# Optimization experiments

Hardware: AMD Instinct MI355X
Metric: run time of the kernel (lower is better)

## Reference

```python
import jax, jax.numpy as jnp
import numpy as np

N, NW, M, H, C = 16384, 512, 32, 8, 16
T_SEG, N_SIG = 512, 3


def _forward(query_feats, key_feats, value_feats, query_table, key_table,
             value_table, table_offsets, win_indices, table_idx):
    # gather voxels into windows: [nW, M, H, C]
    q = query_feats[win_indices]
    k = key_feats[win_indices]
    v = value_feats[win_indices]
    # base attention coefficients: [nW, H, M, M]
    logits = jnp.einsum('wihc,wjhc->whij', q, k)
    n_sig = table_idx.shape[-1]
    for s in range(n_sig):  # fixed, small signal loop (xyz cRSE)
        idx_s = table_offsets[s] + table_idx[..., s]      # [nW, M, M]
        tq = query_table[idx_s]                            # [nW, M, M, H, C]
        tk = key_table[idx_s]
        logits = logits + jnp.einsum('wihc,wijhc->whij', q, tq) \
                        + jnp.einsum('wjhc,wijhc->whij', k, tk)
    # max-stabilized exp (cal_max_coffs + self_attn_forward)
    rmax = jnp.max(logits, axis=-1, keepdims=True)
    ecoff = jnp.exp(logits - rmax)                         # [nW, H, M, M]
    sum_coffs = jnp.sum(ecoff, axis=-1)                    # [nW, H, M]
    raw = jnp.einsum('whij,wjhc->wihc', ecoff, v)          # [nW, M, H, C]
    for s in range(n_sig):
        idx_s = table_offsets[s] + table_idx[..., s]
        tv = value_table[idx_s]
        raw = raw + jnp.einsum('whij,wijhc->wihc', ecoff, tv)
    norm = raw / jnp.transpose(sum_coffs, (0, 2, 1))[..., None]
    # scatter windows back to voxel order (win_indices is a permutation)
    out = jnp.zeros_like(query_feats).at[win_indices.reshape(-1)].set(
        norm.reshape(-1, norm.shape[-2], norm.shape[-1]))
    return out


def setup_inputs() -> dict:
    key = jax.random.key(0)
    ks = jax.random.split(key, 9)
    feats = lambda k: jax.random.normal(k, (N, H, C), dtype=jnp.float32)
    table = lambda k: 0.02 * jax.random.normal(k, (N_SIG * T_SEG, H, C), dtype=jnp.float32)
    win_indices = jax.random.permutation(ks[6], N).reshape(NW, M).astype(jnp.int32)
    table_idx = jax.random.randint(ks[7], (NW, M, M, N_SIG), 0, T_SEG, dtype=jnp.int32)
    table_offsets = (jnp.arange(N_SIG, dtype=jnp.int32) * T_SEG)
    return {
        'query_feats': feats(ks[0]), 'key_feats': feats(ks[1]), 'value_feats': feats(ks[2]),
        'query_table': table(ks[3]), 'key_table': table(ks[4]), 'value_table': table(ks[5]),
        'table_offsets': table_offsets, 'win_indices': win_indices, 'table_idx': table_idx,
    }


def reference(query_feats, key_feats, value_feats, query_table, key_table,
              value_table, table_offsets, win_indices, table_idx):
    return _forward(query_feats, key_feats, value_feats, query_table, key_table,
                    value_table, table_offsets, win_indices, table_idx)
```

## Files before the change

kernel.cpp:

```cpp
#include <hip/hip_runtime.h>

namespace {
constexpr int NWIN = 512;
constexpr int M    = 32;
constexpr int H    = 8;
constexpr int C    = 16;
constexpr int NSIG = 3;
constexpr int HC   = H * C;
constexpr int HB   = 4;
constexpr int HBC  = HB * C;
}

__device__ __forceinline__ float dot4(const float4& a, const float4& b) {
  return a.x * b.x + a.y * b.y + a.z * b.z + a.w * b.w;
}
__device__ __forceinline__ const float4* f4p(const float* p) {
  return reinterpret_cast<const float4*>(p);
}

__global__ __launch_bounds__(256, 4)
void win_attn(const float* __restrict__ qf, const float* __restrict__ kf,
              const float* __restrict__ vf, const float* __restrict__ qt,
              const float* __restrict__ kt, const float* __restrict__ vt,
              const int* __restrict__ toff, const int* __restrict__ widx,
              const int* __restrict__ tidx, float* __restrict__ out)
{
  const int w  = blockIdx.x >> 1;
  const int hb = (blockIdx.x & 1) * HB;
  const int t  = threadIdx.x;
  const int hl = t >> 6;
  const int ch = (t >> 5) & 1;
  const int i  = t & 31;
  const int h  = hb + hl;
  const int cb = ch * 8;

  __shared__ float k_lds[M][HBC];
  __shared__ float v_lds[M][HBC];
  __shared__ int   tid_lds[M * NSIG * M];
  __shared__ int   vox_lds[M];
  __shared__ int   off_lds[NSIG];

  if (t < M)    vox_lds[t] = widx[w * M + t];
  if (t < NSIG) off_lds[t] = toff[t];
  __syncthreads();

  #pragma unroll
  for (int r = 0; r < 2; ++r) {
    const int flat = t + 256 * r;
    const int j    = flat >> 4;
    const int f4i  = (flat & 15) * 4;
    const int goff = vox_lds[j] * HC + hb * C + f4i;
    *reinterpret_cast<float4*>(&k_lds[j][f4i]) = *f4p(kf + goff);
    *reinterpret_cast<float4*>(&v_lds[j][f4i]) = *f4p(vf + goff);
  }
  #pragma unroll
  for (int r = 0; r < 12; ++r) {
    const int g   = t + 256 * r;
    const int ii  = g / 96;
    const int rem = g - ii * 96;
    const int jj  = rem / 3;
    const int ss  = rem - jj * 3;
    tid_lds[(jj * NSIG + ss) * M + ii] = tidx[w * (M * M * NSIG) + g];
  }

  const int vox_i = vox_lds[i];
  const float* qrow = qf + vox_i * HC + h * C + cb;
  const float4 q0 = f4p(qrow)[0], q1 = f4p(qrow)[1];
  const int offs[NSIG] = { off_lds[0], off_lds[1], off_lds[2] };
  __syncthreads();

  float m    = -INFINITY;
  float ssum = 0.f;
  float oacc[8];
  #pragma unroll
  for (int c = 0; c < 8; ++c) oacc[c] = 0.f;

  #pragma unroll
  for (int j = 0; j < M; ++j) {
    const float* krow = &k_lds[j][hl * C + cb];
    const float4 k0 = f4p(krow)[0], k1 = f4p(krow)[1];
    const float4 vv0 = f4p(&v_lds[j][hl * C + cb])[0];
    const float4 vv1 = f4p(&v_lds[j][hl * C + cb])[1];

    float logit = dot4(q0, k0) + dot4(q1, k1);
    float4 tv0[NSIG], tv1[NSIG];
    #pragma unroll
    for (int s = 0; s < NSIG; ++s) {
      const int row = offs[s] + tid_lds[(j * NSIG + s) * M + i];
      const float* base = qt + row * HC + h * C + cb;
      const float4 a0 = f4p(base)[0], a1 = f4p(base)[1];
      const float* kbase = kt + row * HC + h * C + cb;
      const float4 b0 = f4p(kbase)[0], b1 = f4p(kbase)[1];
      const float* vbase = vt + row * HC + h * C + cb;
      tv0[s] = f4p(vbase)[0];
      tv1[s] = f4p(vbase)[1];
      logit += dot4(q0, a0) + dot4(q1, a1) + dot4(k0, b0) + dot4(k1, b1);
    }
    logit += __shfl_xor(logit, 32);

    const float mnew  = fmaxf(m, logit);
    const float scale = expf(m - mnew);
    const float e     = expf(logit - mnew);
    ssum = ssum * scale + e;
    m    = mnew;

    float4 sv0 = tv0[0], sv1 = tv1[0];
    sv0.x += tv0[1].x + tv0[2].x + vv0.x;  sv0.y += tv0[1].y + tv0[2].y + vv0.y;
    sv0.z += tv0[1].z + tv0[2].z + vv0.z;  sv0.w += tv0[1].w + tv0[2].w + vv0.w;
    sv1.x += tv1[1].x + tv1[2].x + vv1.x;  sv1.y += tv1[1].y + tv1[2].y + vv1.y;
    sv1.z += tv1[1].z + tv1[2].z + vv1.z;  sv1.w += tv1[1].w + tv1[2].w + vv1.w;

    oacc[0] = oacc[0] * scale + e * sv0.x;
    oacc[1] = oacc[1] * scale + e * sv0.y;
    oacc[2] = oacc[2] * scale + e * sv0.z;
    oacc[3] = oacc[3] * scale + e * sv0.w;
    oacc[4] = oacc[4] * scale + e * sv1.x;
    oacc[5] = oacc[5] * scale + e * sv1.y;
    oacc[6] = oacc[6] * scale + e * sv1.z;
    oacc[7] = oacc[7] * scale + e * sv1.w;
  }

  const float inv = 1.0f / ssum;
  float* orow = out + vox_i * HC + h * C + cb;
  float4 o0, o1;
  o0.x = oacc[0] * inv;  o0.y = oacc[1] * inv;
  o0.z = oacc[2] * inv;  o0.w = oacc[3] * inv;
  o1.x = oacc[4] * inv;  o1.y = oacc[5] * inv;
  o1.z = oacc[6] * inv;  o1.w = oacc[7] * inv;
  reinterpret_cast<float4*>(orow)[0] = o0;
  reinterpret_cast<float4*>(orow)[1] = o1;
}

extern "C" void kernel_launch(void* const* d_in, const int* in_sizes, int n_in,
                              void* d_out, int out_size, void* d_ws, size_t ws_size,
                              hipStream_t stream) {
  (void)in_sizes; (void)n_in; (void)d_ws; (void)ws_size; (void)out_size;
  const float* qf  = (const float*)d_in[0];
  const float* kf  = (const float*)d_in[1];
  const float* vf  = (const float*)d_in[2];
  const float* qt  = (const float*)d_in[3];
  const float* kt  = (const float*)d_in[4];
  const float* vt  = (const float*)d_in[5];
  const int*  toff = (const int*)d_in[6];
  const int*  widx = (const int*)d_in[7];
  const int*  tidx = (const int*)d_in[8];
  float* out = (float*)d_out;
  win_attn<<<NWIN * 2, 256, 0, stream>>>(qf, kf, vf, qt, kt, vt, toff, widx, tidx, out);
}
```

Before: 351.7 us.

## Double-buffer gathered table rows in registers across key iterations

Splits the per-key loop into a load phase and a consume phase. Each step issues the table-row gathers for the next key into a second register buffer before working on the current key, so global-memory latency overlaps with the arithmetic. To make room for the two 18-float4 buffers, the launch bound drops from 4 to 2 waves-per-SIMD hint, which allows more registers per thread but risks lower occupancy.

```diff
diff --git a/kernel.cpp b/kernel.cpp
--- a/kernel.cpp
+++ b/kernel.cpp
@@ -18,7 +18,9 @@
   return reinterpret_cast<const float4*>(p);
 }
 
-__global__ __launch_bounds__(256, 4)
+struct RowBuf { float4 d[18]; };
+
+__global__ __launch_bounds__(256, 2)
 void win_attn(const float* __restrict__ qf, const float* __restrict__ kf,
               const float* __restrict__ vf, const float* __restrict__ qt,
               const float* __restrict__ kt, const float* __restrict__ vt,
@@ -33,6 +35,8 @@
   const int i  = t & 31;
   const int h  = hb + hl;
   const int cb = ch * 8;
+  const int hcb = h * C + cb;
+  const int lcb = hl * C + cb;
 
   __shared__ float k_lds[M][HBC];
   __shared__ float v_lds[M][HBC];
@@ -64,7 +68,7 @@
   }
 
   const int vox_i = vox_lds[i];
-  const float* qrow = qf + vox_i * HC + h * C + cb;
+  const float* qrow = qf + vox_i * HC + hcb;
   const float4 q0 = f4p(qrow)[0], q1 = f4p(qrow)[1];
   const int offs[NSIG] = { off_lds[0], off_lds[1], off_lds[2] };
   __syncthreads();
@@ -75,26 +79,30 @@
   #pragma unroll
   for (int c = 0; c < 8; ++c) oacc[c] = 0.f;
 
-  #pragma unroll
-  for (int j = 0; j < M; ++j) {
-    const float* krow = &k_lds[j][hl * C + cb];
-    const float4 k0 = f4p(krow)[0], k1 = f4p(krow)[1];
-    const float4 vv0 = f4p(&v_lds[j][hl * C + cb])[0];
-    const float4 vv1 = f4p(&v_lds[j][hl * C + cb])[1];
-
-    float logit = dot4(q0, k0) + dot4(q1, k1);
-    float4 tv0[NSIG], tv1[NSIG];
+  auto load_rows = [&](RowBuf& b, int j) {
     #pragma unroll
     for (int s = 0; s < NSIG; ++s) {
       const int row = offs[s] + tid_lds[(j * NSIG + s) * M + i];
-      const float* base = qt + row * HC + h * C + cb;
-      const float4 a0 = f4p(base)[0], a1 = f4p(base)[1];
-      const float* kbase = kt + row * HC + h * C + cb;
-      const float4 b0 = f4p(kbase)[0], b1 = f4p(kbase)[1];
-      const float* vbase = vt + row * HC + h * C + cb;
-      tv0[s] = f4p(vbase)[0];
-      tv1[s] = f4p(vbase)[1];
-      logit += dot4(q0, a0) + dot4(q1, a1) + dot4(k0, b0) + dot4(k1, b1);
+      const float* bq = qt + row * HC + hcb;
+      const float* bk = kt + row * HC + hcb;
+      const float* bv = vt + row * HC + hcb;
+      b.d[s * 6 + 0] = f4p(bq)[0];  b.d[s * 6 + 1] = f4p(bq)[1];
+      b.d[s * 6 + 2] = f4p(bk)[0];  b.d[s * 6 + 3] = f4p(bk)[1];
+      b.d[s * 6 + 4] = f4p(bv)[0];  b.d[s * 6 + 5] = f4p(bv)[1];
+    }
+  };
+
+  auto consume = [&](const RowBuf& b, int j) {
+    const float* krow = &k_lds[j][lcb];
+    const float4 k0 = f4p(krow)[0], k1 = f4p(krow)[1];
+    const float* vrow = &v_lds[j][lcb];
+    const float4 vv0 = f4p(vrow)[0], vv1 = f4p(vrow)[1];
+
+    float logit = dot4(q0, k0) + dot4(q1, k1);
+    #pragma unroll
+    for (int s = 0; s < NSIG; ++s) {
+      logit += dot4(q0, b.d[s * 6 + 0]) + dot4(q1, b.d[s * 6 + 1])
+             + dot4(k0, b.d[s * 6 + 2]) + dot4(k1, b.d[s * 6 + 3]);
     }
     logit += __shfl_xor(logit, 32);
 
@@ -104,12 +112,14 @@
     ssum = ssum * scale + e;
     m    = mnew;
 
-    float4 sv0 = tv0[0], sv1 = tv1[0];
-    sv0.x += tv0[1].x + tv0[2].x + vv0.x;  sv0.y += tv0[1].y + tv0[2].y + vv0.y;
-    sv0.z += tv0[1].z + tv0[2].z + vv0.z;  sv0.w += tv0[1].w + tv0[2].w + vv0.w;
-    sv1.x += tv1[1].x + tv1[2].x + vv1.x;  sv1.y += tv1[1].y + tv1[2].y + vv1.y;
-    sv1.z += tv1[1].z + tv1[2].z + vv1.z;  sv1.w += tv1[1].w + tv1[2].w + vv1.w;
-
+    float4 sv0 = vv0, sv1 = vv1;
+    #pragma unroll
+    for (int s = 0; s < NSIG; ++s) {
+      sv0.x += b.d[s * 6 + 4].x;  sv0.y += b.d[s * 6 + 4].y;
+      sv0.z += b.d[s * 6 + 4].z;  sv0.w += b.d[s * 6 + 4].w;
+      sv1.x += b.d[s * 6 + 5].x;  sv1.y += b.d[s * 6 + 5].y;
+      sv1.z += b.d[s * 6 + 5].z;  sv1.w += b.d[s * 6 + 5].w;
+    }
     oacc[0] = oacc[0] * scale + e * sv0.x;
     oacc[1] = oacc[1] * scale + e * sv0.y;
     oacc[2] = oacc[2] * scale + e * sv0.z;
@@ -118,10 +128,20 @@
     oacc[5] = oacc[5] * scale + e * sv1.y;
     oacc[6] = oacc[6] * scale + e * sv1.z;
     oacc[7] = oacc[7] * scale + e * sv1.w;
+  };
+
+  RowBuf A, B;
+  load_rows(A, 0);
+  #pragma unroll
+  for (int jj = 0; jj < M / 2; ++jj) {
+    load_rows(B, 2 * jj + 1);
+    consume(A, 2 * jj);
+    if (jj < M / 2 - 1) load_rows(A, 2 * jj + 2);
+    consume(B, 2 * jj + 1);
   }
 
   const float inv = 1.0f / ssum;
-  float* orow = out + vox_i * HC + h * C + cb;
+  float* orow = out + vox_i * HC + hcb;
   float4 o0, o1;
   o0.x = oacc[0] * inv;  o0.y = oacc[1] * inv;
   o0.z = oacc[2] * inv;  o0.w = oacc[3] * inv;
```

Result: slower. 1.185 ms (+236.9%).

## Split key loop across two waves per head with LDS softmax merge

Applied to the files above, without the earlier changes.

Doubles the block to 512 threads so each head/channel-half pair uses two waves, and each wave processes half of the 32 keys with its own online softmax. The partial max, sum and accumulators are merged through shared memory before the write. This is meant to raise the number of threads in flight and shorten each thread's serial chain of latency-bound table gathers. In exchange it adds an extra LDS buffer, a barrier and extra exps, and the launch bounds ask for higher occupancy, which may limit registers.

```diff
diff --git a/kernel.cpp b/kernel.cpp
--- a/kernel.cpp
+++ b/kernel.cpp
@@ -9,6 +9,7 @@
 constexpr int HC   = H * C;
 constexpr int HB   = 4;
 constexpr int HBC  = HB * C;
+constexpr int MS   = 11;
 }
 
 __device__ __forceinline__ float dot4(const float4& a, const float4& b) {
@@ -18,25 +19,30 @@
   return reinterpret_cast<const float4*>(p);
 }
 
-__global__ __launch_bounds__(256, 4)
+__global__ __launch_bounds__(512, 8)
 void win_attn(const float* __restrict__ qf, const float* __restrict__ kf,
               const float* __restrict__ vf, const float* __restrict__ qt,
               const float* __restrict__ kt, const float* __restrict__ vt,
               const int* __restrict__ toff, const int* __restrict__ widx,
               const int* __restrict__ tidx, float* __restrict__ out)
 {
-  const int w  = blockIdx.x >> 1;
-  const int hb = (blockIdx.x & 1) * HB;
-  const int t  = threadIdx.x;
-  const int hl = t >> 6;
-  const int ch = (t >> 5) & 1;
-  const int i  = t & 31;
-  const int h  = hb + hl;
-  const int cb = ch * 8;
+  const int w    = blockIdx.x >> 1;
+  const int hb   = (blockIdx.x & 1) * HB;
+  const int t    = threadIdx.x;
+  const int wave = t >> 6;
+  const int hl   = wave >> 1;
+  const int jh   = wave & 1;
+  const int ch   = (t >> 5) & 1;
+  const int i    = t & 31;
+  const int h    = hb + hl;
+  const int cb   = ch * 8;
+  const int hcb  = h * C + cb;
+  const int lcb  = hl * C + cb;
 
   __shared__ float k_lds[M][HBC];
   __shared__ float v_lds[M][HBC];
   __shared__ int   tid_lds[M * NSIG * M];
+  __shared__ float merge_lds[4 * 2 * 32 * MS];
   __shared__ int   vox_lds[M];
   __shared__ int   off_lds[NSIG];
 
@@ -44,18 +50,16 @@
   if (t < NSIG) off_lds[t] = toff[t];
   __syncthreads();
 
-  #pragma unroll
-  for (int r = 0; r < 2; ++r) {
-    const int flat = t + 256 * r;
-    const int j    = flat >> 4;
-    const int f4i  = (flat & 15) * 4;
+  {
+    const int j   = t >> 4;
+    const int f4i = (t & 15) * 4;
     const int goff = vox_lds[j] * HC + hb * C + f4i;
     *reinterpret_cast<float4*>(&k_lds[j][f4i]) = *f4p(kf + goff);
     *reinterpret_cast<float4*>(&v_lds[j][f4i]) = *f4p(vf + goff);
   }
   #pragma unroll
-  for (int r = 0; r < 12; ++r) {
-    const int g   = t + 256 * r;
+  for (int r = 0; r < 6; ++r) {
+    const int g   = t + 512 * r;
     const int ii  = g / 96;
     const int rem = g - ii * 96;
     const int jj  = rem / 3;
@@ -64,7 +68,7 @@
   }
 
   const int vox_i = vox_lds[i];
-  const float* qrow = qf + vox_i * HC + h * C + cb;
+  const float* qrow = qf + vox_i * HC + hcb;
   const float4 q0 = f4p(qrow)[0], q1 = f4p(qrow)[1];
   const int offs[NSIG] = { off_lds[0], off_lds[1], off_lds[2] };
   __syncthreads();
@@ -75,23 +79,25 @@
   #pragma unroll
   for (int c = 0; c < 8; ++c) oacc[c] = 0.f;
 
+  const int jbase = jh * (M / 2);
   #pragma unroll
-  for (int j = 0; j < M; ++j) {
-    const float* krow = &k_lds[j][hl * C + cb];
+  for (int jr = 0; jr < M / 2; ++jr) {
+    const int j = jbase + jr;
+    const float* krow = &k_lds[j][lcb];
     const float4 k0 = f4p(krow)[0], k1 = f4p(krow)[1];
-    const float4 vv0 = f4p(&v_lds[j][hl * C + cb])[0];
-    const float4 vv1 = f4p(&v_lds[j][hl * C + cb])[1];
+    const float4 vv0 = f4p(&v_lds[j][lcb])[0];
+    const float4 vv1 = f4p(&v_lds[j][lcb])[1];
 
     float logit = dot4(q0, k0) + dot4(q1, k1);
     float4 tv0[NSIG], tv1[NSIG];
     #pragma unroll
     for (int s = 0; s < NSIG; ++s) {
       const int row = offs[s] + tid_lds[(j * NSIG + s) * M + i];
-      const float* base = qt + row * HC + h * C + cb;
+      const float* base = qt + row * HC + hcb;
       const float4 a0 = f4p(base)[0], a1 = f4p(base)[1];
-      const float* kbase = kt + row * HC + h * C + cb;
+      const float* kbase = kt + row * HC + hcb;
       const float4 b0 = f4p(kbase)[0], b1 = f4p(kbase)[1];
-      const float* vbase = vt + row * HC + h * C + cb;
+      const float* vbase = vt + row * HC + hcb;
       tv0[s] = f4p(vbase)[0];
       tv1[s] = f4p(vbase)[1];
       logit += dot4(q0, a0) + dot4(q1, a1) + dot4(k0, b0) + dot4(k1, b1);
@@ -120,15 +126,35 @@
     oacc[7] = oacc[7] * scale + e * sv1.w;
   }
 
-  const float inv = 1.0f / ssum;
-  float* orow = out + vox_i * HC + h * C + cb;
-  float4 o0, o1;
-  o0.x = oacc[0] * inv;  o0.y = oacc[1] * inv;
-  o0.z = oacc[2] * inv;  o0.w = oacc[3] * inv;
-  o1.x = oacc[4] * inv;  o1.y = oacc[5] * inv;
-  o1.z = oacc[6] * inv;  o1.w = oacc[7] * inv;
-  reinterpret_cast<float4*>(orow)[0] = o0;
-  reinterpret_cast<float4*>(orow)[1] = o1;
+  const int slot = ((hl * 2 + ch) * 32 + i) * MS;
+  if (jh == 1) {
+    merge_lds[slot + 0] = m;
+    merge_lds[slot + 1] = ssum;
+    #pragma unroll
+    for (int c = 0; c < 8; ++c) merge_lds[slot + 2 + c] = oacc[c];
+  }
+  __syncthreads();
+  if (jh == 0) {
+    const float m1 = merge_lds[slot + 0];
+    const float s1 = merge_lds[slot + 1];
+    const float Mx = fmaxf(m, m1);
+    const float a  = expf(m - Mx);
+    const float b  = expf(m1 - Mx);
+    const float S  = ssum * a + s1 * b;
+    const float inv = 1.0f / S;
+    float* orow = out + vox_i * HC + hcb;
+    float4 o0, o1;
+    o0.x = (oacc[0] * a + merge_lds[slot + 2] * b) * inv;
+    o0.y = (oacc[1] * a + merge_lds[slot + 3] * b) * inv;
+    o0.z = (oacc[2] * a + merge_lds[slot + 4] * b) * inv;
+    o0.w = (oacc[3] * a + merge_lds[slot + 5] * b) * inv;
+    o1.x = (oacc[4] * a + merge_lds[slot + 6] * b) * inv;
+    o1.y = (oacc[5] * a + merge_lds[slot + 7] * b) * inv;
+    o1.z = (oacc[6] * a + merge_lds[slot + 8] * b) * inv;
+    o1.w = (oacc[7] * a + merge_lds[slot + 9] * b) * inv;
+    reinterpret_cast<float4*>(orow)[0] = o0;
+    reinterpret_cast<float4*>(orow)[1] = o1;
+  }
 }
 
 extern "C" void kernel_launch(void* const* d_in, const int* in_sizes, int n_in,
@@ -145,5 +171,5 @@
   const int*  widx = (const int*)d_in[7];
   const int*  tidx = (const int*)d_in[8];
   float* out = (float*)d_out;
-  win_attn<<<NWIN * 2, 256, 0, stream>>>(qf, kf, vf, qt, kt, vt, toff, widx, tidx, out);
+  win_attn<<<NWIN * 2, 512, 0, stream>>>(qf, kf, vf, qt, kt, vt, toff, widx, tidx, out);
 }
```

Measured after the change: 1.011 ms. 187% more time.
